# Kernel tuning notes

Measured on AMD Instinct MI355X. Metric: run time of the kernel, lower is better.

Reference implementation:

```python
import jax, jax.numpy as jnp
import numpy as np
import math

DIM = 1024
N_HEADS = 16
N_KV_HEADS = 8
HEAD_DIM = 64
HIDDEN = 4096
WINDOW = 512
NORM_EPS = 1e-5
QK_EPS = 1e-6


def get_alibi_slopes(n_heads):
    def _power_of_2(n):
        start = 2 ** (-2 ** (-(math.log2(n) - 3)))
        return [start * start ** i for i in range(n)]
    if math.log2(n_heads).is_integer():
        return _power_of_2(n_heads)
    closest = 2 ** math.floor(math.log2(n_heads))
    slopes = _power_of_2(closest)
    extra = _power_of_2(2 * closest)
    slopes.extend(extra[0::2][:n_heads - closest])
    return slopes


def layer_norm(x, w, eps):
    m = x.mean(-1, keepdims=True)
    v = ((x - m) ** 2).mean(-1, keepdims=True)
    return (x - m) * jax.lax.rsqrt(v + eps) * w


def setup_inputs() -> dict:
    key = jax.random.key(0)
    ks = jax.random.split(key, 16)
    s = 0.02
    return {
        "x": jax.random.normal(ks[0], (2, 2048, DIM), dtype=jnp.float32),
        "wq": jax.random.normal(ks[1], (N_HEADS * HEAD_DIM, DIM), dtype=jnp.float32) * s,
        "wk": jax.random.normal(ks[2], (N_KV_HEADS * HEAD_DIM, DIM), dtype=jnp.float32) * s,
        "wv": jax.random.normal(ks[3], (N_KV_HEADS * HEAD_DIM, DIM), dtype=jnp.float32) * s,
        "wo": jax.random.normal(ks[4], (DIM, N_HEADS * HEAD_DIM), dtype=jnp.float32) * s,
        "q_norm_w": jnp.ones((N_HEADS * HEAD_DIM,), dtype=jnp.float32),
        "k_norm_w": jnp.ones((N_KV_HEADS * HEAD_DIM,), dtype=jnp.float32),
        "attn_norm_w": jnp.ones((DIM,), dtype=jnp.float32),
        "ffn_norm_w": jnp.ones((DIM,), dtype=jnp.float32),
        "w1": jax.random.normal(ks[5], (HIDDEN, DIM), dtype=jnp.float32) * s,
        "w2": jax.random.normal(ks[6], (DIM, HIDDEN), dtype=jnp.float32) * s,
        "w3": jax.random.normal(ks[7], (HIDDEN, DIM), dtype=jnp.float32) * s,
        "attn_scale": jnp.full((DIM,), 1e-5, dtype=jnp.float32),
        "ffn_scale": jnp.full((DIM,), 1e-5, dtype=jnp.float32),
    }


def reference(x, wq, wk, wv, wo, q_norm_w, k_norm_w, attn_norm_w, ffn_norm_w,
              w1, w2, w3, attn_scale, ffn_scale):
    bsz, seqlen, _ = x.shape
    n_rep = N_HEADS // N_KV_HEADS

    h = layer_norm(x, attn_norm_w, NORM_EPS)
    q = layer_norm(h @ wq.T, q_norm_w, QK_EPS).reshape(bsz, seqlen, N_HEADS, HEAD_DIM).transpose(0, 2, 1, 3)
    k = layer_norm(h @ wk.T, k_norm_w, QK_EPS).reshape(bsz, seqlen, N_KV_HEADS, HEAD_DIM).transpose(0, 2, 1, 3)
    v = (h @ wv.T).reshape(bsz, seqlen, N_KV_HEADS, HEAD_DIM).transpose(0, 2, 1, 3)
    k = jnp.repeat(k, n_rep, axis=1)  # [b, H, s, hd]
    v = jnp.repeat(v, n_rep, axis=1)

    pos = jnp.arange(seqlen)
    dist = pos[None, :] - pos[:, None]  # dist[i, j] = j - i (as in the torch code)
    base = jnp.where((dist >= 0) & (dist <= WINDOW), 0.0, -jnp.inf)  # [s, s]
    slopes = jnp.asarray(get_alibi_slopes(N_HEADS), dtype=jnp.float32)
    alibi = -jnp.abs(slopes[:, None, None] * dist.astype(jnp.float32))  # [H, s, s]
    full_mask = base[None, :, :] + alibi  # [H, s, s]

    scores = jnp.einsum('bhqd,bhkd->bhqk', q, k) / math.sqrt(HEAD_DIM) + full_mask[None]
    attn = jax.nn.softmax(scores, axis=-1)
    out = jnp.einsum('bhqk,bhkd->bhqd', attn, v)
    out = out.transpose(0, 2, 1, 3).reshape(bsz, seqlen, N_HEADS * HEAD_DIM)
    x = x + (out @ wo.T) * attn_scale

    h2 = layer_norm(x, ffn_norm_w, NORM_EPS)
    ffn = (jax.nn.silu(h2 @ w1.T) * (h2 @ w3.T)) @ w2.T
    return x + ffn * ffn_scale
```

## Files before the change

### kernel.cpp

```cpp
#include <hip/hip_runtime.h>


typedef __bf16 bf16;
typedef __attribute__((ext_vector_type(8))) __bf16 bf16x8;
typedef __attribute__((ext_vector_type(4))) float f32x4;
typedef __attribute__((ext_vector_type(4))) short s16x4;

#define MFMA16(a, b, c) __builtin_amdgcn_mfma_f32_16x16x32_bf16(a, b, c, 0, 0, 0)

__device__ __forceinline__ void gload_lds16(const bf16* g, bf16* l) {
    __builtin_amdgcn_global_load_lds(
        (const __attribute__((address_space(1))) unsigned int*)g,
        (__attribute__((address_space(3))) unsigned int*)l, 16, 0, 0);
}

__global__ void sniff_kernel(const unsigned short* __restrict__ x, int* __restrict__ flag) {
    __shared__ int s;
    if (threadIdx.x == 0) s = 0;
    __syncthreads();
    int bad = 0;
#pragma unroll
    for (int i = 0; i < 16; ++i) {
        const unsigned short u = x[threadIdx.x * 16 + i];
        const int e = (u >> 7) & 0xFF;
        if (e >= 135) bad = 1;
    }
    if (bad) atomicOr(&s, 1);
    __syncthreads();
    if (threadIdx.x == 0) flag[0] = s;
}

__global__ void convert_all_kernel(const void* __restrict__ wq, const void* __restrict__ wk,
                                   const void* __restrict__ wv, const void* __restrict__ wo,
                                   const void* __restrict__ w1, const void* __restrict__ w3,
                                   const void* __restrict__ w2, bf16* __restrict__ dst,
                                   const int* __restrict__ flag) {
    const long e = ((long)blockIdx.x * 256 + threadIdx.x) * 4;
    const void* src; long off;
    if      (e < 1048576)  { src = wq; off = 0; }
    else if (e < 1572864)  { src = wk; off = 1048576; }
    else if (e < 2097152)  { src = wv; off = 1572864; }
    else if (e < 3145728)  { src = wo; off = 2097152; }
    else if (e < 7340032)  { src = w1; off = 3145728; }
    else if (e < 11534336) { src = w3; off = 7340032; }
    else                   { src = w2; off = 11534336; }
    if (flag[0] != 0) {
        const f32x4 v = *(const f32x4*)((const float*)src + (e - off));
        bf16 tmp[4];
#pragma unroll
        for (int j = 0; j < 4; ++j) tmp[j] = (bf16)v[j];
        *(s16x4*)(dst + e) = *(s16x4*)tmp;
    } else {
        *(s16x4*)(dst + e) = *(const s16x4*)((const short*)src + (e - off));
    }
}

__global__ void ln_kernel(const void* __restrict__ in, const void* __restrict__ w,
                          bf16* __restrict__ out, int W, float eps,
                          const int* __restrict__ flag, int in_flv, int w_flv) {
    const int row = blockIdx.x, t = threadIdx.x;
    const int nch = W >> 3;
    const bool act = t < nch;
    const bool f32 = flag[0] != 0;
    float v[8];
    float s = 0.f, s2 = 0.f;
    if (act) {
        if (in_flv && f32) {
            const float* rp = (const float*)in + (size_t)row * W + t * 8;
            const f32x4 a = *(const f32x4*)rp, b = *(const f32x4*)(rp + 4);
#pragma unroll
            for (int j = 0; j < 4; ++j) { v[j] = a[j]; v[4 + j] = b[j]; }
        } else {
            const bf16x8 xv = *(const bf16x8*)((const bf16*)in + (size_t)row * W + t * 8);
#pragma unroll
            for (int j = 0; j < 8; ++j) v[j] = (float)xv[j];
        }
#pragma unroll
        for (int j = 0; j < 8; ++j) { s += v[j]; s2 += v[j] * v[j]; }
    }
#pragma unroll
    for (int off = 32; off; off >>= 1) { s += __shfl_xor(s, off); s2 += __shfl_xor(s2, off); }
    __shared__ float red[4];
    if ((t & 63) == 0) { red[(t >> 6) * 2] = s; red[(t >> 6) * 2 + 1] = s2; }
    __syncthreads();
    const float fs = red[0] + red[2], fs2 = red[1] + red[3];
    const float inw = 1.f / (float)W;
    const float mean = fs * inw;
    const float var = fs2 * inw - mean * mean;
    const float rstd = rsqrtf(var + eps);
    if (act) {
        float wv8[8];
        if (w_flv && f32) {
            const float* wp = (const float*)w + t * 8;
            const f32x4 a = *(const f32x4*)wp, b = *(const f32x4*)(wp + 4);
#pragma unroll
            for (int j = 0; j < 4; ++j) { wv8[j] = a[j]; wv8[4 + j] = b[j]; }
        } else {
            const bf16x8 ww = *(const bf16x8*)((const bf16*)w + t * 8);
#pragma unroll
            for (int j = 0; j < 8; ++j) wv8[j] = (float)ww[j];
        }
        bf16x8 ov;
#pragma unroll
        for (int j = 0; j < 8; ++j) ov[j] = (bf16)((v[j] - mean) * rstd * wv8[j]);
        *(bf16x8*)(out + (size_t)row * W + t * 8) = ov;
    }
}

__global__ void reduce_k(const bf16* __restrict__ p, const bf16* __restrict__ x1,
                         const void* __restrict__ scale, void* __restrict__ out,
                         const int* __restrict__ flag) {
    const bool f32 = flag[0] != 0;
    const size_t i8 = ((size_t)blockIdx.x * 256 + threadIdx.x) * 8;
    const int col = (int)(i8 & 1023);
    const bf16x8 a = *(const bf16x8*)(p + i8);
    const bf16x8 b = *(const bf16x8*)(p + 4194304 + i8);
    const bf16x8 r = *(const bf16x8*)(x1 + i8);
    float sc8[8];
    if (f32) {
        const f32x4 s0 = *(const f32x4*)((const float*)scale + col);
        const f32x4 s1 = *(const f32x4*)((const float*)scale + col + 4);
#pragma unroll
        for (int j = 0; j < 4; ++j) { sc8[j] = s0[j]; sc8[4 + j] = s1[j]; }
    } else {
        const bf16x8 sb = *(const bf16x8*)((const bf16*)scale + col);
#pragma unroll
        for (int j = 0; j < 8; ++j) sc8[j] = (float)sb[j];
    }
    float o[8];
#pragma unroll
    for (int j = 0; j < 8; ++j)
        o[j] = (float)r[j] + ((float)a[j] + (float)b[j]) * sc8[j];
    if (f32) {
        f32x4 o0, o1;
#pragma unroll
        for (int j = 0; j < 4; ++j) { o0[j] = o[j]; o1[j] = o[4 + j]; }
        *(f32x4*)((float*)out + i8) = o0;
        *(f32x4*)((float*)out + i8 + 4) = o1;
    } else {
        bf16x8 ov;
#pragma unroll
        for (int j = 0; j < 8; ++j) ov[j] = (bf16)o[j];
        *(bf16x8*)((bf16*)out + i8) = ov;
    }
}

template <int EPI, int NBUF, int SWZ, int SPLITK>
__global__ __launch_bounds__(512, 4)
void gemm2(const bf16* __restrict__ A, const bf16* __restrict__ B,
           void* __restrict__ Cout, const void* __restrict__ res,
           const void* __restrict__ scale, int M, int N, int K,
           const int* __restrict__ flag, int res_flv, int out_flv) {
    __shared__ bf16 LDS[NBUF * 8192];
    const bool f32 = flag[0] != 0;
    const int t = threadIdx.x;
    const int wv = t >> 6, ln = t & 63;
    const int qr = ln & 15, g = ln >> 4;
    const int wr = wv >> 2, wc = wv & 3;
    int bx = blockIdx.x, by = blockIdx.y;
    if (SWZ) {
        const int bid = by * gridDim.x + bx;
        const int g8 = bid & 7, m = bid >> 3;
        bx = m % gridDim.x;
        by = g8 + 8 * (m / gridDim.x);
    }
    const int row0 = by * 128, col0 = bx * 128;

    const int Koff = SPLITK ? (int)blockIdx.z * (K >> 1) : 0;
    const int Keff = SPLITK ? (K >> 1) : K;
    if (SPLITK) Cout = (void*)((bf16*)Cout + (size_t)blockIdx.z * ((size_t)M * N));

    f32x4 acc[4][2] = {};

    const int cx = ((t & 3) ^ ((t >> 2) & 3)) * 8;
    const bf16* aSrc = A + (size_t)(row0 + (t >> 2)) * K + Koff + cx;
    const bf16* bSrc = B + (size_t)(col0 + (t >> 2)) * K + Koff + cx;
    const int gx8 = (g ^ (qr & 3)) * 8;
    const int NIT = Keff >> 5;

#define STAGE(bi, k0)                                              \
    do {                                                           \
        bf16* lb = LDS + (bi) * 8192 + wv * 512;                   \
        gload_lds16(aSrc + (k0), lb);                              \
        gload_lds16(bSrc + (k0), lb + 4096);                       \
    } while (0)

#pragma unroll
    for (int pb = 0; pb < NBUF - 1; ++pb) STAGE(pb, pb * 32);
    if constexpr (NBUF == 3) asm volatile("s_waitcnt vmcnt(2)" ::: "memory");
    else                     asm volatile("s_waitcnt vmcnt(6)" ::: "memory");
    __builtin_amdgcn_s_barrier();
    __builtin_amdgcn_sched_barrier(0);

    int cur = 0, sb = NBUF - 1;
    for (int it = 0; it < NIT; ++it) {
        const bool more = (it + NBUF - 1) < NIT;
        if (more) STAGE(sb, (it + NBUF - 1) * 32);
        const bf16* bufA = LDS + cur * 8192;
        const bf16* bufB = bufA + 4096;
        bf16x8 af[4], bfr[2];
#pragma unroll
        for (int i = 0; i < 4; ++i)
            af[i] = *(const bf16x8*)&bufA[(wr * 64 + i * 16 + qr) * 32 + gx8];
#pragma unroll
        for (int j = 0; j < 2; ++j)
            bfr[j] = *(const bf16x8*)&bufB[(wc * 32 + j * 16 + qr) * 32 + gx8];
#pragma unroll
        for (int i = 0; i < 4; ++i)
#pragma unroll
            for (int j = 0; j < 2; ++j)
                acc[i][j] = MFMA16(af[i], bfr[j], acc[i][j]);
        if (more) {
            if constexpr (NBUF == 3) asm volatile("s_waitcnt vmcnt(2)" ::: "memory");
            else                     asm volatile("s_waitcnt vmcnt(6)" ::: "memory");
        } else {
            asm volatile("s_waitcnt vmcnt(0)" ::: "memory");
        }
        __builtin_amdgcn_s_barrier();
        __builtin_amdgcn_sched_barrier(0);
        cur = cur + 1 == NBUF ? 0 : cur + 1;
        sb  = sb + 1 == NBUF ? 0 : sb + 1;
    }
#undef STAGE

#pragma unroll
    for (int i = 0; i < 4; ++i) {
#pragma unroll
        for (int j = 0; j < 2; ++j) {
            const int rr0 = row0 + wr * 64 + i * 16 + g * 4;
            const int cc  = col0 + wc * 32 + j * 16 + qr;
            if (EPI == 4) {
                if (cc < 1024) {
#pragma unroll
                    for (int r = 0; r < 4; ++r)
                        ((bf16*)Cout)[(size_t)(rr0 + r) * 1024 + cc] = (bf16)acc[i][j][r];
                } else if (cc < 1536) {
#pragma unroll
                    for (int r = 0; r < 4; ++r)
                        ((bf16*)res)[(size_t)(rr0 + r) * 512 + (cc - 1024)] = (bf16)acc[i][j][r];
                } else {
                    const int kv = cc - 1536, kvh = kv >> 6, d = kv & 63;
                    const int bb = rr0 >> 11, s0 = rr0 & 2047;
                    bf16 tmp[4];
#pragma unroll
                    for (int r = 0; r < 4; ++r) tmp[r] = (bf16)acc[i][j][r];
                    *(s16x4*)((bf16*)scale + (((size_t)bb * 8 + kvh) * 64 + d) * 2048 + s0) = *(s16x4*)tmp;
                }
            } else {
                float scv = 0.f;
                if (EPI == 1)
                    scv = f32 ? ((const float*)scale)[cc] : (float)((const bf16*)scale)[cc];
#pragma unroll
                for (int r = 0; r < 4; ++r) {
                    const size_t idx = (size_t)(rr0 + r) * N + cc;
                    float vv = acc[i][j][r];
                    if (EPI == 1) {
                        const float rv = (res_flv && f32) ? ((const float*)res)[idx]
                                                          : (float)((const bf16*)res)[idx];
                        vv = rv + vv * scv;
                    }
                    if (EPI == 3) {
                        const float uv = (float)((const bf16*)res)[idx];
                        vv = uv / (1.f + __expf(-uv)) * vv;
                    }
                    if (out_flv && f32) ((float*)Cout)[idx] = vv;
                    else                ((bf16*)Cout)[idx] = (bf16)vv;
                }
            }
        }
    }
}

template <int EPI>
__global__ __launch_bounds__(512, 4)
void gemm3(const bf16* __restrict__ A, const bf16* __restrict__ B,
           bf16* __restrict__ C, const bf16* __restrict__ res,
           int M, int N, int K) {
    __shared__ bf16 LDS[3 * 12288];
    const int t = threadIdx.x;
    const int wv = t >> 6, ln = t & 63;
    const int qr = ln & 15, g = ln >> 4;
    const int wr = wv >> 1, wc = wv & 1;
    const int row0 = blockIdx.y * 256, col0 = blockIdx.x * 128;

    f32x4 acc[4][4] = {};

    const int cx = ((t & 3) ^ ((t >> 2) & 3)) * 8;
    const bf16* aSrc  = A + (size_t)(row0 + (t >> 2)) * K + cx;
    const bf16* aSrc2 = A + (size_t)(row0 + 128 + (t >> 2)) * K + cx;
    const bf16* bSrc  = B + (size_t)(col0 + (t >> 2)) * K + cx;
    const int gx8 = (g ^ (qr & 3)) * 8;
    const int NIT = K >> 5;

#define STAGE3(bi, k0)                                             \
    do {                                                           \
        bf16* lb = LDS + (bi) * 12288 + wv * 512;                  \
        gload_lds16(aSrc + (k0), lb);                              \
        gload_lds16(aSrc2 + (k0), lb + 4096);                      \
        gload_lds16(bSrc + (k0), lb + 8192);                       \
    } while (0)

    STAGE3(0, 0);
    STAGE3(1, 32);
    asm volatile("s_waitcnt vmcnt(3)" ::: "memory");
    __builtin_amdgcn_s_barrier();
    __builtin_amdgcn_sched_barrier(0);

    int cur = 0, sb = 2;
    for (int it = 0; it < NIT; ++it) {
        const bool more = (it + 2) < NIT;
        if (more) STAGE3(sb, (it + 2) * 32);
        const bf16* bufA = LDS + cur * 12288;
        const bf16* bufB = bufA + 8192;
        bf16x8 af[4], bfr[4];
#pragma unroll
        for (int i = 0; i < 4; ++i)
            af[i] = *(const bf16x8*)&bufA[(wr * 64 + i * 16 + qr) * 32 + gx8];
#pragma unroll
        for (int j = 0; j < 4; ++j)
            bfr[j] = *(const bf16x8*)&bufB[(wc * 64 + j * 16 + qr) * 32 + gx8];
#pragma unroll
        for (int i = 0; i < 4; ++i)
#pragma unroll
            for (int j = 0; j < 4; ++j)
                acc[i][j] = MFMA16(bfr[j], af[i], acc[i][j]);
        if (more) asm volatile("s_waitcnt vmcnt(3)" ::: "memory");
        else      asm volatile("s_waitcnt vmcnt(0)" ::: "memory");
        __builtin_amdgcn_s_barrier();
        __builtin_amdgcn_sched_barrier(0);
        cur = cur == 2 ? 0 : cur + 1;
        sb  = sb  == 2 ? 0 : sb  + 1;
    }
#undef STAGE3

#pragma unroll
    for (int i = 0; i < 4; ++i) {
        const int row = row0 + wr * 64 + i * 16 + qr;
#pragma unroll
        for (int j = 0; j < 4; ++j) {
            const int col = col0 + wc * 64 + j * 16 + g * 4;
            const size_t idx = (size_t)row * N + col;
            bf16 tmp[4];
            if (EPI == 3) {
                const s16x4 rv4 = *(const s16x4*)(res + idx);
#pragma unroll
                for (int r = 0; r < 4; ++r) {
                    bf16 ub; *(short*)&ub = rv4[r];
                    const float uv = (float)ub;
                    tmp[r] = (bf16)(uv / (1.f + __expf(-uv)) * acc[i][j][r]);
                }
            } else {
#pragma unroll
                for (int r = 0; r < 4; ++r) tmp[r] = (bf16)acc[i][j][r];
            }
            *(s16x4*)(C + idx) = *(s16x4*)tmp;
        }
    }
}

__global__ __launch_bounds__(256)
void attn_kernel(const bf16* __restrict__ qn, const bf16* __restrict__ kn,
                 const bf16* __restrict__ vt, bf16* __restrict__ aout) {
    __shared__ bf16 SH[3 * 4096];
    const int t = threadIdx.x, wv = t >> 6, ln = t & 63;
    const int qr = ln & 15, g = ln >> 4;
    const int h = blockIdx.y, b = blockIdx.z, kvh = h >> 1;
    const int q0blk = blockIdx.x * 64;
    const int qa = q0blk + wv * 16 + qr;
    const float slope = exp2f(-0.5f * (float)(h + 1));

    const bf16* qrow = qn + ((size_t)(b * 2048 + qa)) * 1024 + h * 64;
    const bf16x8 qb0 = *(const bf16x8*)(qrow + g * 8);
    const bf16x8 qb1 = *(const bf16x8*)(qrow + 32 + g * 8);

    const bf16* kbase = kn + (size_t)b * 2048 * 512 + kvh * 64;
    const bf16* vbase = vt + ((size_t)(b * 8 + kvh) * 64) * 2048;
    const int krow_l = t >> 3;
    const int kcsrc  = (t & 7) ^ ((t >> 3) & 7);
    const int vd     = t >> 2;
    const int vcsrc  = (t & 3) ^ ((t >> 2) & 3);
    const bf16* kgsrc = kbase + kcsrc * 8;
    const bf16* vgsrc = vbase + (size_t)vd * 2048;
    bf16* lK0 = SH + wv * 512;
    bf16* lV0 = SH + 2048 + wv * 512;

#define STAGE_T(kts, bi)                                           \
    do {                                                           \
        int ksrc = (kts) + krow_l;                                 \
        ksrc = ksrc > 2047 ? 2047 : ksrc;                          \
        gload_lds16(kgsrc + (size_t)ksrc * 512, lK0 + (bi) * 4096);\
        int vsrc = (kts) + vcsrc * 8;                              \
        vsrc = vsrc > 2040 ? 2040 : vsrc;                          \
        gload_lds16(vgsrc + vsrc, lV0 + (bi) * 4096);              \
    } while (0)

    STAGE_T(q0blk, 0);
    STAGE_T(q0blk + 32, 1);
    asm volatile("s_waitcnt vmcnt(2)" ::: "memory");
    __builtin_amdgcn_s_barrier();
    __builtin_amdgcn_sched_barrier(0);

    f32x4 o[4] = {};
    float mrun = -1e29f, lsum = 0.f;
    int cur = 0, sb = 2;

    for (int it = 0; it < 18; ++it) {
        const int kt = q0blk + it * 32;
        const bool more = (it + 2) < 18;
        if (more) STAGE_T(kt + 64, sb);
        const bf16* Kb = SH + cur * 4096;
        const bf16* Vb = Kb + 2048;

        f32x4 sc[2] = {f32x4{0, 0, 0, 0}, f32x4{0, 0, 0, 0}};
#pragma unroll
        for (int ks = 0; ks < 2; ++ks) {
            const int lrow = ks * 16 + qr;
            const int sw = (lrow & 7) * 8;
            sc[ks] = MFMA16(*(const bf16x8*)&Kb[lrow * 64 + (((g) * 8) ^ sw)],        qb0, sc[ks]);
            sc[ks] = MFMA16(*(const bf16x8*)&Kb[lrow * 64 + (((4 + g) * 8) ^ sw)],    qb1, sc[ks]);
        }
        float s[2][4], p[2][4];
        float tmax = -1e30f;
#pragma unroll
        for (int ks = 0; ks < 2; ++ks)
#pragma unroll
            for (int r = 0; r < 4; ++r) {
                const int key = kt + ks * 16 + g * 4 + r;
                const int dist = key - qa;
                const bool valid = (dist >= 0) && (dist <= 512) && (key < 2048);
                const float sv = valid ? sc[ks][r] * 0.125f - slope * (float)dist : -1e30f;
                s[ks][r] = sv;
                tmax = fmaxf(tmax, sv);
            }
        tmax = fmaxf(tmax, __shfl_xor(tmax, 16));
        tmax = fmaxf(tmax, __shfl_xor(tmax, 32));
        const float mnew = fmaxf(mrun, tmax);
        const float alpha = __expf(mrun - mnew);
        mrun = mnew;
        float ps = 0.f;
#pragma unroll
        for (int ks = 0; ks < 2; ++ks)
#pragma unroll
            for (int r = 0; r < 4; ++r) { p[ks][r] = __expf(s[ks][r] - mnew); ps += p[ks][r]; }
        lsum = lsum * alpha + ps;
#pragma unroll
        for (int fd = 0; fd < 4; ++fd) o[fd] *= alpha;

        bf16x8 pb;
#pragma unroll
        for (int j = 0; j < 8; ++j) {
            const int srcl = (((2 * g + (j >> 2)) & 3) << 4) | qr;
            const float v0 = __shfl(p[0][j & 3], srcl);
            const float v1 = __shfl(p[1][j & 3], srcl);
            pb[j] = (bf16)((g & 2) ? v1 : v0);
        }
#pragma unroll
        for (int fd = 0; fd < 4; ++fd) {
            const int d = fd * 16 + qr;
            const bf16x8 va = *(const bf16x8*)&Vb[d * 32 + ((g ^ (d & 3)) * 8)];
            o[fd] = MFMA16(va, pb, o[fd]);
        }

        if (more) asm volatile("s_waitcnt vmcnt(2)" ::: "memory");
        else      asm volatile("s_waitcnt vmcnt(0)" ::: "memory");
        __builtin_amdgcn_s_barrier();
        __builtin_amdgcn_sched_barrier(0);
        cur = cur == 2 ? 0 : cur + 1;
        sb  = sb  == 2 ? 0 : sb  + 1;
    }
#undef STAGE_T

    float lt = lsum + __shfl_xor(lsum, 16);
    lt += __shfl_xor(lt, 32);
    lt = fmaxf(lt, 1e-30f);
    const float inv = 1.f / lt;
    bf16* orow = aout + ((size_t)(b * 2048 + qa)) * 1024 + h * 64;
#pragma unroll
    for (int fd = 0; fd < 4; ++fd) {
        bf16 tmp[4];
#pragma unroll
        for (int r = 0; r < 4; ++r) tmp[r] = (bf16)(o[fd][r] * inv);
        *(s16x4*)(orow + fd * 16 + g * 4) = *(s16x4*)tmp;
    }
}

extern "C" void kernel_launch(void* const* d_in, const int* in_sizes, int n_in,
                              void* d_out, int out_size, void* d_ws, size_t ws_size,
                              hipStream_t stream) {
    int* flag = (int*)d_ws;
    bf16* base = (bf16*)d_ws + 64;
    bf16* h    = base;
    bf16* q    = h + 4194304;
    bf16* kbuf = q + 4194304;
    bf16* vtb  = kbuf + 2097152;
    bf16* aout = vtb + 2097152;
    bf16* u    = aout + 4194304;
    bf16* wcv  = u + 16777216;

    bf16* woc = wcv + 2097152;
    bf16* w1c = wcv + 3145728;
    bf16* w3c = wcv + 7340032;
    bf16* w2c = wcv + 11534336;

    const dim3 blk(512);
    sniff_kernel<<<1, 256, 0, stream>>>((const unsigned short*)d_in[0], flag);
    convert_all_kernel<<<15360, 256, 0, stream>>>(
        d_in[1], d_in[2], d_in[3], d_in[4], d_in[9], d_in[11], d_in[10], wcv, flag);

    ln_kernel<<<4096, 128, 0, stream>>>(d_in[0], d_in[7], h, 1024, 1e-5f, flag, 1, 1);
    gemm2<4, 3, 0, 0><<<dim3(16, 32), blk, 0, stream>>>(h, wcv, q, kbuf, vtb, 4096, 2048, 1024, flag, 0, 0);
    ln_kernel<<<4096, 128, 0, stream>>>(q, d_in[5], q, 1024, 1e-6f, flag, 0, 1);
    ln_kernel<<<4096, 128, 0, stream>>>(kbuf, d_in[6], kbuf, 512, 1e-6f, flag, 0, 1);
    attn_kernel<<<dim3(32, 16, 2), dim3(256), 0, stream>>>(q, kbuf, vtb, aout);
    gemm2<1, 3, 1, 0><<<dim3(8, 32), blk, 0, stream>>>(aout, woc, q, d_in[0], d_in[12], 4096, 1024, 1024, flag, 1, 0);
    ln_kernel<<<4096, 128, 0, stream>>>(q, d_in[8], h, 1024, 1e-5f, flag, 0, 1);
    gemm3<0><<<dim3(32, 16), blk, 0, stream>>>(h, w1c, u, nullptr, 4096, 4096, 1024);
    gemm3<3><<<dim3(32, 16), blk, 0, stream>>>(h, w3c, u, u,       4096, 4096, 1024);
    gemm2<0, 5, 1, 1><<<dim3(8, 32, 2), blk, 0, stream>>>(u, w2c, kbuf, nullptr, nullptr, 4096, 1024, 4096, flag, 0, 0);
    reduce_k<<<2048, 256, 0, stream>>>(kbuf, q, d_in[13], d_out, flag);
}
```

Before: 267.1 us.

## Fuse w1 and w3 FFN GEMMs into one kernel with SiLU-gate epilogue

Replaces the two separate gemm3 launches for w1 and w3 with a single kernel. Each block loads one A tile and both B1 and B3 tiles, keeps two accumulators and applies silu(u1)*u3 in the epilogue. This avoids writing u out and reading it back, and avoids reloading the activation tile. It also adds grouped block-index swizzling for L2 locality. The epilogue now stores scalar bf16 values with a column-per-lane layout, which is less coalesced than the previous vector stores.

```diff
diff --git a/kernel.cpp b/kernel.cpp
--- a/kernel.cpp
+++ b/kernel.cpp
@@ -271,37 +271,43 @@
     }
 }
 
-template <int EPI>
 __global__ __launch_bounds__(512, 4)
-void gemm3(const bf16* __restrict__ A, const bf16* __restrict__ B,
-           bf16* __restrict__ C, const bf16* __restrict__ res,
-           int M, int N, int K) {
+void gemm_w13(const bf16* __restrict__ A, const bf16* __restrict__ B1,
+              const bf16* __restrict__ B3, bf16* __restrict__ C,
+              int M, int N, int K) {
     __shared__ bf16 LDS[3 * 12288];
     const int t = threadIdx.x;
     const int wv = t >> 6, ln = t & 63;
     const int qr = ln & 15, g = ln >> 4;
-    const int wr = wv >> 1, wc = wv & 1;
-    const int row0 = blockIdx.y * 256, col0 = blockIdx.x * 128;
-
-    f32x4 acc[4][4] = {};
+    const int wr = wv >> 2, wc = wv & 3;
+    int bx = blockIdx.x, by = blockIdx.y;
+    {
+        const int bid = by * gridDim.x + bx;
+        const int g8 = bid & 7, m = bid >> 3;
+        bx = m % gridDim.x;
+        by = g8 + 8 * (m / gridDim.x);
+    }
+    const int row0 = by * 128, col0 = bx * 128;
+
+    f32x4 acc1[4][2] = {}, acc3[4][2] = {};
 
     const int cx = ((t & 3) ^ ((t >> 2) & 3)) * 8;
-    const bf16* aSrc  = A + (size_t)(row0 + (t >> 2)) * K + cx;
-    const bf16* aSrc2 = A + (size_t)(row0 + 128 + (t >> 2)) * K + cx;
-    const bf16* bSrc  = B + (size_t)(col0 + (t >> 2)) * K + cx;
+    const bf16* aSrc  = A  + (size_t)(row0 + (t >> 2)) * K + cx;
+    const bf16* b1Src = B1 + (size_t)(col0 + (t >> 2)) * K + cx;
+    const bf16* b3Src = B3 + (size_t)(col0 + (t >> 2)) * K + cx;
     const int gx8 = (g ^ (qr & 3)) * 8;
     const int NIT = K >> 5;
 
-#define STAGE3(bi, k0)                                             \
+#define STAGEW(bi, k0)                                             \
     do {                                                           \
         bf16* lb = LDS + (bi) * 12288 + wv * 512;                  \
         gload_lds16(aSrc + (k0), lb);                              \
-        gload_lds16(aSrc2 + (k0), lb + 4096);                      \
-        gload_lds16(bSrc + (k0), lb + 8192);                       \
+        gload_lds16(b1Src + (k0), lb + 4096);                      \
+        gload_lds16(b3Src + (k0), lb + 8192);                      \
     } while (0)
 
-    STAGE3(0, 0);
-    STAGE3(1, 32);
+    STAGEW(0, 0);
+    STAGEW(1, 32);
     asm volatile("s_waitcnt vmcnt(3)" ::: "memory");
     __builtin_amdgcn_s_barrier();
     __builtin_amdgcn_sched_barrier(0);
@@ -309,21 +315,26 @@
     int cur = 0, sb = 2;
     for (int it = 0; it < NIT; ++it) {
         const bool more = (it + 2) < NIT;
-        if (more) STAGE3(sb, (it + 2) * 32);
-        const bf16* bufA = LDS + cur * 12288;
-        const bf16* bufB = bufA + 8192;
-        bf16x8 af[4], bfr[4];
+        if (more) STAGEW(sb, (it + 2) * 32);
+        const bf16* bufA  = LDS + cur * 12288;
+        const bf16* bufB1 = bufA + 4096;
+        const bf16* bufB3 = bufA + 8192;
+        bf16x8 af[4], b1f[2], b3f[2];
 #pragma unroll
         for (int i = 0; i < 4; ++i)
             af[i] = *(const bf16x8*)&bufA[(wr * 64 + i * 16 + qr) * 32 + gx8];
 #pragma unroll
-        for (int j = 0; j < 4; ++j)
-            bfr[j] = *(const bf16x8*)&bufB[(wc * 64 + j * 16 + qr) * 32 + gx8];
+        for (int j = 0; j < 2; ++j) {
+            b1f[j] = *(const bf16x8*)&bufB1[(wc * 32 + j * 16 + qr) * 32 + gx8];
+            b3f[j] = *(const bf16x8*)&bufB3[(wc * 32 + j * 16 + qr) * 32 + gx8];
+        }
 #pragma unroll
         for (int i = 0; i < 4; ++i)
 #pragma unroll
-            for (int j = 0; j < 4; ++j)
-                acc[i][j] = MFMA16(bfr[j], af[i], acc[i][j]);
+            for (int j = 0; j < 2; ++j) {
+                acc1[i][j] = MFMA16(af[i], b1f[j], acc1[i][j]);
+                acc3[i][j] = MFMA16(af[i], b3f[j], acc3[i][j]);
+            }
         if (more) asm volatile("s_waitcnt vmcnt(3)" ::: "memory");
         else      asm volatile("s_waitcnt vmcnt(0)" ::: "memory");
         __builtin_amdgcn_s_barrier();
@@ -331,29 +342,20 @@
         cur = cur == 2 ? 0 : cur + 1;
         sb  = sb  == 2 ? 0 : sb  + 1;
     }
-#undef STAGE3
+#undef STAGEW
 
 #pragma unroll
     for (int i = 0; i < 4; ++i) {
-        const int row = row0 + wr * 64 + i * 16 + qr;
-#pragma unroll
-        for (int j = 0; j < 4; ++j) {
-            const int col = col0 + wc * 64 + j * 16 + g * 4;
-            const size_t idx = (size_t)row * N + col;
-            bf16 tmp[4];
-            if (EPI == 3) {
-                const s16x4 rv4 = *(const s16x4*)(res + idx);
-#pragma unroll
-                for (int r = 0; r < 4; ++r) {
-                    bf16 ub; *(short*)&ub = rv4[r];
-                    const float uv = (float)ub;
-                    tmp[r] = (bf16)(uv / (1.f + __expf(-uv)) * acc[i][j][r]);
-                }
-            } else {
-#pragma unroll
-                for (int r = 0; r < 4; ++r) tmp[r] = (bf16)acc[i][j][r];
+#pragma unroll
+        for (int j = 0; j < 2; ++j) {
+            const int rr0 = row0 + wr * 64 + i * 16 + g * 4;
+            const int cc  = col0 + wc * 32 + j * 16 + qr;
+#pragma unroll
+            for (int r = 0; r < 4; ++r) {
+                const float u1 = acc1[i][j][r];
+                const float u3 = acc3[i][j][r];
+                C[(size_t)(rr0 + r) * N + cc] = (bf16)(u1 / (1.f + __expf(-u1)) * u3);
             }
-            *(s16x4*)(C + idx) = *(s16x4*)tmp;
         }
     }
 }
@@ -514,8 +516,7 @@
     attn_kernel<<<dim3(32, 16, 2), dim3(256), 0, stream>>>(q, kbuf, vtb, aout);
     gemm2<1, 3, 1, 0><<<dim3(8, 32), blk, 0, stream>>>(aout, woc, q, d_in[0], d_in[12], 4096, 1024, 1024, flag, 1, 0);
     ln_kernel<<<4096, 128, 0, stream>>>(q, d_in[8], h, 1024, 1e-5f, flag, 0, 1);
-    gemm3<0><<<dim3(32, 16), blk, 0, stream>>>(h, w1c, u, nullptr, 4096, 4096, 1024);
-    gemm3<3><<<dim3(32, 16), blk, 0, stream>>>(h, w3c, u, u,       4096, 4096, 1024);
+    gemm_w13<<<dim3(32, 32), blk, 0, stream>>>(h, w1c, w3c, u, 4096, 4096, 1024);
     gemm2<0, 5, 1, 1><<<dim3(8, 32, 2), blk, 0, stream>>>(u, w2c, kbuf, nullptr, nullptr, 4096, 1024, 4096, flag, 0, 0);
     reduce_k<<<2048, 256, 0, stream>>>(kbuf, q, d_in[13], d_out, flag);
 }
```

New measurement: 262.2 us. Within noise of the previous version (-1.9%).
